# Performance work log

Measured on AMD Instinct MI355X. Metric: run time of the kernel, lower is better.

## Reference

```python
import jax, jax.numpy as jnp
import numpy as np

D = 768          # wav2vec2-base hidden size
H = 4            # cross-attn heads
HD = D // H
B = 8
N = 1024         # w2v sequence length (target length)
T = 2000         # raw CQCC frames
N_GAT = 3
NUM_CLASSES = 2


def _p(key, shape, scale=0.02):
    return jax.random.normal(key, shape, dtype=jnp.float32) * scale


def layer_norm(x, g, b, eps=1e-5):
    m = x.mean(-1, keepdims=True)
    v = x.var(-1, keepdims=True)
    return (x - m) * jax.lax.rsqrt(v + eps) * g + b


def gelu(x):
    return jax.nn.gelu(x, approximate=False)


def conv1d(x, w, b):
    # x [B,C,T], w [O,I,K], padding=1 (same)
    y = jax.lax.conv_general_dilated(x, w, (1,), [(1, 1)], dimension_numbers=('NCH', 'OIH', 'NCH'))
    return y + b[None, :, None]


def batchnorm(x, g, b, m, v, eps=1e-5):
    # eval-mode BatchNorm1d on [B,C,T]
    return (x - m[None, :, None]) * jax.lax.rsqrt(v[None, :, None] + eps) * g[None, :, None] + b[None, :, None]


def interp_linear(x, target_len):
    # torch F.interpolate(mode='linear', align_corners=False); x [B,T,D] -> [B,target_len,D]
    t_in = x.shape[1]
    pos = (jnp.arange(target_len, dtype=jnp.float32) + 0.5) * (t_in / target_len) - 0.5
    pos = jnp.clip(pos, 0.0, t_in - 1.0)
    lo = jnp.floor(pos).astype(jnp.int32)
    hi = jnp.minimum(lo + 1, t_in - 1)
    w = (pos - lo.astype(jnp.float32))[None, :, None]
    return x[:, lo] * (1.0 - w) + x[:, hi] * w


def mha(q, k, v, in_w, in_b, out_w, out_b):
    # torch nn.MultiheadAttention, batch_first=True
    bb, nq, _ = q.shape
    nk = k.shape[1]
    wq, wk, wv = in_w[:D], in_w[D:2 * D], in_w[2 * D:]
    bq, bk, bv = in_b[:D], in_b[D:2 * D], in_b[2 * D:]
    qh = (q @ wq.T + bq).reshape(bb, nq, H, HD).transpose(0, 2, 1, 3)
    kh = (k @ wk.T + bk).reshape(bb, nk, H, HD).transpose(0, 2, 1, 3)
    vh = (v @ wv.T + bv).reshape(bb, nk, H, HD).transpose(0, 2, 1, 3)
    scores = jnp.einsum('bhqd,bhkd->bhqk', qh, kh) * (1.0 / np.sqrt(HD))
    alpha = jax.nn.softmax(scores, axis=-1)
    o = jnp.einsum('bhqk,bhkd->bhqd', alpha, vh).transpose(0, 2, 1, 3).reshape(bb, nq, D)
    return o @ out_w.T + out_b


def graph_attn(x, fc_w, fc_b, a_w, a_b):
    # GAT score on concat([h_i, h_j]) decomposes additively: e_ij = a_i.h_i + a_j.h_j + b
    h = x @ fc_w.T + fc_b                      # [B,N,D]
    s_i = h @ a_w[:D]                          # [B,N]
    s_j = h @ a_w[D:]                          # [B,N]
    e = s_i[:, :, None] + s_j[:, None, :] + a_b  # [B,N,N]
    alpha = jax.nn.softmax(e, axis=-1)
    return jnp.einsum('bij,bjd->bid', alpha, h)


def _forward(w2v, cqcc, conv1_w, conv1_b, bn1_g, bn1_b, bn1_m, bn1_v,
             conv2_w, conv2_b, bn2_g, bn2_b, bn2_m, bn2_v, pos_embed,
             lnq_g, lnq_b, lnkv_g, lnkv_b,
             a1_in_w, a1_in_b, a1_out_w, a1_out_b,
             a2_in_w, a2_in_b, a2_out_w, a2_out_b,
             gat_fc_w, gat_fc_b, gat_a_w, gat_a_b, gln_g, gln_b,
             clf_w1, clf_b1, clf_w2, clf_b2):
    # CQCC conv stack
    x = gelu(batchnorm(conv1d(cqcc, conv1_w, conv1_b), bn1_g, bn1_b, bn1_m, bn1_v))
    x = gelu(batchnorm(conv1d(x, conv2_w, conv2_b), bn2_g, bn2_b, bn2_m, bn2_v))  # [B,D,T]
    cq = interp_linear(x.transpose(0, 2, 1), w2v.shape[1])  # [B,N,D]
    # shared positional encoding
    n = w2v.shape[1]
    w = w2v + pos_embed[:, :n]
    cq = cq + pos_embed[:, :n]
    # bidirectional cross attention (norm_q / norm_kv shared across directions)
    out1 = mha(layer_norm(cq, lnq_g, lnq_b), layer_norm(w, lnkv_g, lnkv_b),
               layer_norm(w, lnkv_g, lnkv_b), a1_in_w, a1_in_b, a1_out_w, a1_out_b)
    out2 = mha(layer_norm(w, lnq_g, lnq_b), layer_norm(cq, lnkv_g, lnkv_b),
               layer_norm(cq, lnkv_g, lnkv_b), a2_in_w, a2_in_b, a2_out_w, a2_out_b)
    x = out1 + out2
    # 3 residual graph-attention blocks
    for l in range(N_GAT):
        res = x
        x = graph_attn(x, gat_fc_w[l], gat_fc_b[l], gat_a_w[l], gat_a_b[l])
        x = layer_norm(x + res, gln_g[l], gln_b[l])
    pooled = x.mean(axis=1)
    h = gelu(pooled @ clf_w1.T + clf_b1)
    return h @ clf_w2.T + clf_b2


def setup_inputs():
    ks = iter(jax.random.split(jax.random.key(0), 64))
    inp = {}
    inp['w2v'] = jax.random.normal(next(ks), (B, N, D), dtype=jnp.float32)
    inp['cqcc'] = jax.random.normal(next(ks), (B, 20, T), dtype=jnp.float32)
    inp['conv1_w'] = _p(next(ks), (128, 20, 3)); inp['conv1_b'] = jnp.zeros((128,), jnp.float32)
    inp['bn1_g'] = jnp.ones((128,), jnp.float32); inp['bn1_b'] = jnp.zeros((128,), jnp.float32)
    inp['bn1_m'] = jnp.zeros((128,), jnp.float32); inp['bn1_v'] = jnp.ones((128,), jnp.float32)
    inp['conv2_w'] = _p(next(ks), (D, 128, 3)); inp['conv2_b'] = jnp.zeros((D,), jnp.float32)
    inp['bn2_g'] = jnp.ones((D,), jnp.float32); inp['bn2_b'] = jnp.zeros((D,), jnp.float32)
    inp['bn2_m'] = jnp.zeros((D,), jnp.float32); inp['bn2_v'] = jnp.ones((D,), jnp.float32)
    inp['pos_embed'] = _p(next(ks), (1, 2000, D), 1.0)
    inp['lnq_g'] = jnp.ones((D,), jnp.float32); inp['lnq_b'] = jnp.zeros((D,), jnp.float32)
    inp['lnkv_g'] = jnp.ones((D,), jnp.float32); inp['lnkv_b'] = jnp.zeros((D,), jnp.float32)
    inp['a1_in_w'] = _p(next(ks), (3 * D, D)); inp['a1_in_b'] = jnp.zeros((3 * D,), jnp.float32)
    inp['a1_out_w'] = _p(next(ks), (D, D)); inp['a1_out_b'] = jnp.zeros((D,), jnp.float32)
    inp['a2_in_w'] = _p(next(ks), (3 * D, D)); inp['a2_in_b'] = jnp.zeros((3 * D,), jnp.float32)
    inp['a2_out_w'] = _p(next(ks), (D, D)); inp['a2_out_b'] = jnp.zeros((D,), jnp.float32)
    inp['gat_fc_w'] = _p(next(ks), (N_GAT, D, D)); inp['gat_fc_b'] = jnp.zeros((N_GAT, D), jnp.float32)
    inp['gat_a_w'] = _p(next(ks), (N_GAT, 2 * D)); inp['gat_a_b'] = jnp.zeros((N_GAT,), jnp.float32)
    inp['gln_g'] = jnp.ones((N_GAT, D), jnp.float32); inp['gln_b'] = jnp.zeros((N_GAT, D), jnp.float32)
    inp['clf_w1'] = _p(next(ks), (128, D)); inp['clf_b1'] = jnp.zeros((128,), jnp.float32)
    inp['clf_w2'] = _p(next(ks), (NUM_CLASSES, 128)); inp['clf_b2'] = jnp.zeros((NUM_CLASSES,), jnp.float32)
    return inp


def reference(w2v, cqcc, conv1_w, conv1_b, bn1_g, bn1_b, bn1_m, bn1_v,
              conv2_w, conv2_b, bn2_g, bn2_b, bn2_m, bn2_v, pos_embed,
              lnq_g, lnq_b, lnkv_g, lnkv_b,
              a1_in_w, a1_in_b, a1_out_w, a1_out_b,
              a2_in_w, a2_in_b, a2_out_w, a2_out_b,
              gat_fc_w, gat_fc_b, gat_a_w, gat_a_b, gln_g, gln_b,
              clf_w1, clf_b1, clf_w2, clf_b2):
    return _forward(w2v, cqcc, conv1_w, conv1_b, bn1_g, bn1_b, bn1_m, bn1_v,
                    conv2_w, conv2_b, bn2_g, bn2_b, bn2_m, bn2_v, pos_embed,
                    lnq_g, lnq_b, lnkv_g, lnkv_b,
                    a1_in_w, a1_in_b, a1_out_w, a1_out_b,
                    a2_in_w, a2_in_b, a2_out_w, a2_out_b,
                    gat_fc_w, gat_fc_b, gat_a_w, gat_a_b, gln_g, gln_b,
                    clf_w1, clf_b1, clf_w2, clf_b2)
```

## Files before the change

### kernel.cpp

```cpp
#include <hip/hip_runtime.h>
#include <math.h>

#define DD 768
#define NH 4
#define HDIM 192
#define BBATCH 8
#define NSEQ 1024
#define TLEN 2000
#define SLOT 6291456
#define XROW 256256

typedef _Float16 h16;
typedef _Float16 half8v __attribute__((ext_vector_type(8)));
typedef _Float16 half4v __attribute__((ext_vector_type(4)));
typedef float f32x4 __attribute__((ext_vector_type(4)));

__device__ __forceinline__ float gelu_f(float x){
  return 0.5f * x * (1.0f + erff(x * 0.70710678118654752440f));
}
__device__ __forceinline__ float wave_sum(float v){
  #pragma unroll
  for (int off = 32; off; off >>= 1) v += __shfl_xor(v, off);
  return v;
}
__device__ __forceinline__ float wave_max(float v){
  #pragma unroll
  for (int off = 32; off; off >>= 1) v = fmaxf(v, __shfl_xor(v, off));
  return v;
}
__device__ __forceinline__ void gload16(const h16* g, h16* l){
  __builtin_amdgcn_global_load_lds(
      (const __attribute__((address_space(1))) void*)g,
      (__attribute__((address_space(3))) void*)l, 16, 0, 0);
}
__device__ __forceinline__ int xcd_remap(int orig, int nwg){
  int q = nwg >> 3, r = nwg & 7;
  int xcd = orig & 7, idx = orig >> 3;
  return (xcd < r ? xcd * (q + 1) : r * (q + 1) + (xcd - r) * q) + idx;
}

struct CastArgs {
  const float* s[5];
  h16* d[5];
  int cum[6];
};
__global__ __launch_bounds__(256) void k_cast5(CastArgs a, int total){
  int i = blockIdx.x * 256 + threadIdx.x;
  if (i >= total) return;
  int seg = 0;
  #pragma unroll
  for (int t = 1; t < 5; ++t) seg += (i >= a.cum[t]);
  int off = i - a.cum[seg];
  a.d[seg][off] = (h16)a.s[seg][off];
}

__global__ __launch_bounds__(256) void k_castc2(const float* __restrict__ s,
    h16* __restrict__ d){
  int i = blockIdx.x * 256 + threadIdx.x;
  if (i >= 294912) return;
  int oc = i / 384, rem = i % 384;
  int ic = rem / 3, kh = rem % 3;
  d[oc * 384 + kh * 128 + ic] = (h16)s[i];
}

__global__ __launch_bounds__(256) void k_conv1t(const float* __restrict__ cqcc,
    const float* __restrict__ w, const float* __restrict__ bias,
    const float* __restrict__ g, const float* __restrict__ be,
    const float* __restrict__ mm, const float* __restrict__ vv,
    h16* __restrict__ X){
  __shared__ float xs[20][258];
  __shared__ float wsm[32*60];
  const int t0 = blockIdx.x * 256;
  const int ocg = blockIdx.y, b = blockIdx.z;
  const int tid = threadIdx.x;
  for (int idx = tid; idx < 20*258; idx += 256){
    int ic = idx / 258, tt = idx % 258;
    int t = t0 + tt - 1;
    xs[ic][tt] = (t >= 0 && t < TLEN) ? cqcc[((size_t)b*20 + ic)*TLEN + t] : 0.f;
  }
  for (int idx = tid; idx < 32*60; idx += 256)
    wsm[idx] = w[ocg*32*60 + idx];
  __syncthreads();
  int t = t0 + tid;
  if (t >= TLEN) return;
  float acc[32] = {};
  for (int ic = 0; ic < 20; ++ic){
    float x0 = xs[ic][tid], x1v = xs[ic][tid+1], x2v = xs[ic][tid+2];
    #pragma unroll
    for (int oc = 0; oc < 32; ++oc){
      const float* wp = &wsm[(oc*20 + ic)*3];
      acc[oc] += wp[0]*x0 + wp[1]*x1v + wp[2]*x2v;
    }
  }
  h16* dst = X + (size_t)b*XROW + (size_t)(t+1)*128 + ocg*32;
  #pragma unroll 4
  for (int oc = 0; oc < 32; ++oc){
    int c = ocg*32 + oc;
    float s = rsqrtf(vv[c] + 1e-5f) * g[c];
    float val = (acc[oc] + bias[c] - mm[c]) * s + be[c];
    dst[oc] = (h16)gelu_f(val);
  }
  if (t == 0){
    h16* z = X + (size_t)b*XROW + ocg*32;
    #pragma unroll
    for (int oc = 0; oc < 32; ++oc) z[oc] = (h16)0.f;
  }
  if (t == TLEN-1){
    h16* z = X + (size_t)b*XROW + (size_t)2001*128 + ocg*32;
    #pragma unroll
    for (int oc = 0; oc < 32; ++oc) z[oc] = (h16)0.f;
  }
}

__global__ void k_bnprep(const float* __restrict__ cb, const float* __restrict__ g,
    const float* __restrict__ be, const float* __restrict__ m,
    const float* __restrict__ v, float* __restrict__ sc, float* __restrict__ off){
  int i = blockIdx.x * 256 + threadIdx.x;
  if (i >= DD) return;
  float s = g[i] * rsqrtf(v[i] + 1e-5f);
  sc[i] = s;
  off[i] = (cb[i] - m[i]) * s + be[i];
}

__global__ __launch_bounds__(256) void k_interp_ln(const h16* __restrict__ x2,
    const float* __restrict__ pe,
    const float* __restrict__ g1, const float* __restrict__ b1, h16* __restrict__ o1,
    const float* __restrict__ g2, const float* __restrict__ b2, h16* __restrict__ o2){
  __shared__ float ss[4], sqq[4];
  int row = blockIdx.x, tid = threadIdx.x;
  int b = row >> 10, i = row & 1023;
  float p = (i + 0.5f) * ((float)TLEN / (float)NSEQ) - 0.5f;
  p = fminf(fmaxf(p, 0.f), (float)(TLEN - 1));
  int lo = (int)floorf(p);
  int hi = min(lo + 1, TLEN - 1);
  float w = p - (float)lo;
  const h16* blo = x2 + ((size_t)b * TLEN + lo) * DD;
  const h16* bhi = x2 + ((size_t)b * TLEN + hi) * DD;
  const float* per = pe + (size_t)i * DD;
  float v[3]; float s = 0.f, sq = 0.f;
  #pragma unroll
  for (int j = 0; j < 3; ++j){
    int d = j * 256 + tid;
    float x = (float)blo[d] * (1.f - w) + (float)bhi[d] * w + per[d];
    v[j] = x; s += x; sq += x * x;
  }
  s = wave_sum(s); sq = wave_sum(sq);
  int wv = tid >> 6;
  if ((tid & 63) == 0){ ss[wv] = s; sqq[wv] = sq; }
  __syncthreads();
  s  = ss[0] + ss[1] + ss[2] + ss[3];
  sq = sqq[0] + sqq[1] + sqq[2] + sqq[3];
  float mean = s * (1.f / DD);
  float var  = sq * (1.f / DD) - mean * mean;
  float r = rsqrtf(var + 1e-5f);
  #pragma unroll
  for (int j = 0; j < 3; ++j){
    int d = j * 256 + tid;
    float xn = (v[j] - mean) * r;
    o1[(size_t)row * DD + d] = (h16)(xn * g1[d] + b1[d]);
    o2[(size_t)row * DD + d] = (h16)(xn * g2[d] + b2[d]);
  }
}

__global__ __launch_bounds__(256) void k_addpos_ln(const float* __restrict__ xin,
    const float* __restrict__ pe,
    const float* __restrict__ g1, const float* __restrict__ b1, h16* __restrict__ o1,
    const float* __restrict__ g2, const float* __restrict__ b2, h16* __restrict__ o2){
  __shared__ float ss[4], sqq[4];
  int row = blockIdx.x, tid = threadIdx.x;
  int i = row & 1023;
  const float* ip = xin + (size_t)row * DD;
  const float* per = pe + (size_t)i * DD;
  float v[3]; float s = 0.f, sq = 0.f;
  #pragma unroll
  for (int j = 0; j < 3; ++j){
    int d = j * 256 + tid;
    float x = ip[d] + per[d];
    v[j] = x; s += x; sq += x * x;
  }
  s = wave_sum(s); sq = wave_sum(sq);
  int wv = tid >> 6;
  if ((tid & 63) == 0){ ss[wv] = s; sqq[wv] = sq; }
  __syncthreads();
  s  = ss[0] + ss[1] + ss[2] + ss[3];
  sq = sqq[0] + sqq[1] + sqq[2] + sqq[3];
  float mean = s * (1.f / DD);
  float var  = sq * (1.f / DD) - mean * mean;
  float r = rsqrtf(var + 1e-5f);
  #pragma unroll
  for (int j = 0; j < 3; ++j){
    int d = j * 256 + tid;
    float xn = (v[j] - mean) * r;
    o1[(size_t)row * DD + d] = (h16)(xn * g1[d] + b1[d]);
    o2[(size_t)row * DD + d] = (h16)(xn * g2[d] + b2[d]);
  }
}

__global__ __launch_bounds__(256) void k_lnH(const h16* __restrict__ in,
    const float* __restrict__ ctx, const float* __restrict__ g,
    const float* __restrict__ be, h16* __restrict__ out){
  __shared__ float ss[4], sqq[4];
  int row = blockIdx.x, tid = threadIdx.x;
  const h16* ip = in + (size_t)row * DD;
  int b = row >> 10;
  float v[3]; float s = 0.f, sq = 0.f;
  #pragma unroll
  for (int j = 0; j < 3; ++j){
    int d = j * 256 + tid;
    float x = (float)ip[d] + ctx[b * DD + d];
    v[j] = x; s += x; sq += x * x;
  }
  s = wave_sum(s); sq = wave_sum(sq);
  int w = tid >> 6;
  if ((tid & 63) == 0){ ss[w] = s; sqq[w] = sq; }
  __syncthreads();
  s  = ss[0] + ss[1] + ss[2] + ss[3];
  sq = sqq[0] + sqq[1] + sqq[2] + sqq[3];
  float mean = s * (1.f / DD);
  float var  = sq * (1.f / DD) - mean * mean;
  float r = rsqrtf(var + 1e-5f);
  #pragma unroll
  for (int j = 0; j < 3; ++j){
    int d = j * 256 + tid;
    out[(size_t)row * DD + d] = (h16)((v[j] - mean) * r * g[d] + be[d]);
  }
}

#define GEMM_MAINLOOP(Abase, lda, Wbase, ldw, Kdim)                          \
  auto stage = [&](int buf, int kt){                                         \
    _Pragma("unroll")                                                        \
    for (int i = 0; i < 4; ++i){                                             \
      int p = i*256 + tid; int row = p >> 3; int ch = (p & 7) ^ (row & 7);   \
      gload16(Abase + (size_t)(m0+row)*lda + kt + ch*8, &Als[buf][p*8]);     \
    }                                                                        \
    _Pragma("unroll")                                                        \
    for (int i = 0; i < 4; ++i){                                             \
      int p = i*256 + tid; int row = p >> 3; int ch = (p & 7) ^ (row & 7);   \
      gload16(Wbase + (size_t)(n0+row)*ldw + kt + ch*8, &Bls[buf][p*8]);     \
    }                                                                        \
  };                                                                         \
  stage(0, 0);                                                               \
  const int nk = Kdim >> 6;                                                  \
  for (int t = 0; t < nk; ++t){                                              \
    const int cur = t & 1;                                                   \
    if (t + 1 < nk){                                                         \
      stage(cur ^ 1, (t + 1) << 6);                                          \
      asm volatile("s_waitcnt vmcnt(8)" ::: "memory");                       \
    } else {                                                                 \
      asm volatile("s_waitcnt vmcnt(0)" ::: "memory");                       \
    }                                                                        \
    __builtin_amdgcn_s_barrier();                                            \
    __builtin_amdgcn_sched_barrier(0);                                       \
    __builtin_amdgcn_s_setprio(1);                                           \
    _Pragma("unroll")                                                        \
    for (int kk = 0; kk < 2; ++kk){                                          \
      half8v af[4], bf[4];                                                   \
      _Pragma("unroll")                                                      \
      for (int mi = 0; mi < 4; ++mi){                                        \
        int row = wr*64 + mi*16 + lr;                                        \
        int chp = (kk*4 + lg) ^ (row & 7);                                   \
        af[mi] = *(const half8v*)&Als[cur][row*64 + chp*8];                  \
      }                                                                      \
      _Pragma("unroll")                                                      \
      for (int ni = 0; ni < 4; ++ni){                                        \
        int row = wc*64 + ni*16 + lr;                                        \
        int chp = (kk*4 + lg) ^ (row & 7);                                   \
        bf[ni] = *(const half8v*)&Bls[cur][row*64 + chp*8];                  \
      }                                                                      \
      _Pragma("unroll")                                                      \
      for (int mi = 0; mi < 4; ++mi)                                         \
        _Pragma("unroll")                                                    \
        for (int ni = 0; ni < 4; ++ni)                                       \
          acc[mi][ni] = __builtin_amdgcn_mfma_f32_16x16x32_f16(              \
              af[mi], bf[ni], acc[mi][ni], 0, 0, 0);                         \
    }                                                                        \
    __builtin_amdgcn_s_setprio(0);                                           \
    asm volatile("s_waitcnt lgkmcnt(0)" ::: "memory");                       \
    __builtin_amdgcn_sched_barrier(0);                                       \
    __builtin_amdgcn_s_barrier();                                            \
  }

__global__ __launch_bounds__(256) void k_gemm_h(
    const h16* __restrict__ A, const h16* __restrict__ W,
    int lda, int ldw, int ldc, int K,
    const float* __restrict__ bias, const float* __restrict__ sc,
    const float* __restrict__ off, const h16* __restrict__ addh,
    float* __restrict__ outf, h16* __restrict__ outh,
    const float* __restrict__ rdw, float* __restrict__ rdpart)
{
  __shared__ h16 Als[2][128*64];
  __shared__ h16 Bls[2][128*64];
  const int tid = threadIdx.x;
  const int gx = gridDim.x, gy = gridDim.y;
  const int wg = xcd_remap(blockIdx.x + gx * blockIdx.y, gx * gy);
  const int nidx = wg % gx;
  const int n0 = nidx * 128, m0 = (wg / gx) * 128;
  const int lane = tid & 63, wid = tid >> 6;
  const int wr = wid >> 1, wc = wid & 1;
  const int lr = lane & 15, lg = lane >> 4;
  f32x4 acc[4][4] = {};
  GEMM_MAINLOOP(A, lda, W, ldw, K)
  float rd[4][4] = {};
  #pragma unroll
  for (int mi = 0; mi < 4; ++mi){
    #pragma unroll
    for (int ni = 0; ni < 4; ++ni){
      int col = n0 + wc*64 + ni*16 + lr;
      int rowb = m0 + wr*64 + mi*16 + lg*4;
      float cb = bias ? bias[col] : 0.f;
      float aw = rdw ? rdw[col] : 0.f;
      #pragma unroll
      for (int r = 0; r < 4; ++r){
        size_t idx = (size_t)(rowb + r) * ldc + col;
        float v = acc[mi][ni][r];
        if (sc){ v = v * sc[col] + off[col]; v = gelu_f(v); }
        else v += cb;
        if (addh) v += (float)addh[idx];
        if (outf) outf[idx] = v;
        if (outh) outh[idx] = (h16)v;
        if (rdw) rd[mi][r] += v * aw;
      }
    }
  }
  if (rdw){
    #pragma unroll
    for (int mi = 0; mi < 4; ++mi){
      #pragma unroll
      for (int r = 0; r < 4; ++r){
        float p = rd[mi][r];
        #pragma unroll
        for (int o = 1; o < 16; o <<= 1) p += __shfl_xor(p, o);
        if (lr == 0){
          int row = m0 + wr*64 + mi*16 + lg*4 + r;
          rdpart[(size_t)row * 12 + nidx*2 + wc] = p;
        }
      }
    }
  }
}

__global__ __launch_bounds__(256) void k_conv2g(
    const h16* __restrict__ X, const h16* __restrict__ W,
    const float* __restrict__ sc, const float* __restrict__ off,
    h16* __restrict__ out)
{
  __shared__ h16 Als[2][128*64];
  __shared__ h16 Bls[2][128*64];
  const int tid = threadIdx.x;
  const int gx = gridDim.x, gy = gridDim.y;
  const int wg = xcd_remap(blockIdx.x + gx * blockIdx.y, gx * gy);
  const int n0 = (wg % gx) * 128, m0 = (wg / gx) * 128;
  const int lane = tid & 63, wid = tid >> 6;
  const int wr = wid >> 1, wc = wid & 1;
  const int lr = lane & 15, lg = lane >> 4;
  f32x4 acc[4][4] = {};
  auto stage = [&](int buf, int kt){
    #pragma unroll
    for (int i = 0; i < 4; ++i){
      int p = i*256 + tid; int row = p >> 3; int ch = (p & 7) ^ (row & 7);
      int rm = m0 + row, b = rm >> 11, t = rm & 2047;
      gload16(X + (size_t)b*XROW + (size_t)t*128 + kt + ch*8, &Als[buf][p*8]);
    }
    #pragma unroll
    for (int i = 0; i < 4; ++i){
      int p = i*256 + tid; int row = p >> 3; int ch = (p & 7) ^ (row & 7);
      gload16(W + (size_t)(n0+row)*384 + kt + ch*8, &Bls[buf][p*8]);
    }
  };
  stage(0, 0);
  const int nk = 6;
  for (int t = 0; t < nk; ++t){
    const int cur = t & 1;
    if (t + 1 < nk){
      stage(cur ^ 1, (t + 1) << 6);
      asm volatile("s_waitcnt vmcnt(8)" ::: "memory");
    } else {
      asm volatile("s_waitcnt vmcnt(0)" ::: "memory");
    }
    __builtin_amdgcn_s_barrier();
    __builtin_amdgcn_sched_barrier(0);
    __builtin_amdgcn_s_setprio(1);
    #pragma unroll
    for (int kk = 0; kk < 2; ++kk){
      half8v af[4], bf[4];
      #pragma unroll
      for (int mi = 0; mi < 4; ++mi){
        int row = wr*64 + mi*16 + lr;
        int chp = (kk*4 + lg) ^ (row & 7);
        af[mi] = *(const half8v*)&Als[cur][row*64 + chp*8];
      }
      #pragma unroll
      for (int ni = 0; ni < 4; ++ni){
        int row = wc*64 + ni*16 + lr;
        int chp = (kk*4 + lg) ^ (row & 7);
        bf[ni] = *(const half8v*)&Bls[cur][row*64 + chp*8];
      }
      #pragma unroll
      for (int mi = 0; mi < 4; ++mi)
        #pragma unroll
        for (int ni = 0; ni < 4; ++ni)
          acc[mi][ni] = __builtin_amdgcn_mfma_f32_16x16x32_f16(
              af[mi], bf[ni], acc[mi][ni], 0, 0, 0);
    }
    __builtin_amdgcn_s_setprio(0);
    asm volatile("s_waitcnt lgkmcnt(0)" ::: "memory");
    __builtin_amdgcn_sched_barrier(0);
    __builtin_amdgcn_s_barrier();
  }
  #pragma unroll
  for (int mi = 0; mi < 4; ++mi){
    #pragma unroll
    for (int ni = 0; ni < 4; ++ni){
      int col = n0 + wc*64 + ni*16 + lr;
      int rowb = m0 + wr*64 + mi*16 + lg*4;
      #pragma unroll
      for (int r = 0; r < 4; ++r){
        int rm = rowb + r, b = rm >> 11, t = rm & 2047;
        if (t < TLEN){
          float v = acc[mi][ni][r] * sc[col] + off[col];
          out[((size_t)b*TLEN + t)*DD + col] = (h16)gelu_f(v);
        }
      }
    }
  }
}

__global__ __launch_bounds__(256) void k_gemm6(
    const h16* __restrict__ Lall, const h16* __restrict__ w6,
    const float* __restrict__ b1, const float* __restrict__ b2,
    h16* __restrict__ qkv6)
{
  __shared__ h16 Als[2][128*64];
  __shared__ h16 Bls[2][128*64];
  const int tid = threadIdx.x;
  const int gx = gridDim.x, gy = gridDim.y;
  const int nwg = gx * gy * 6;
  const int wg = xcd_remap(blockIdx.x + gx*(blockIdx.y + gy*blockIdx.z), nwg);
  const int n0 = (wg % gx) * 128;
  const int m0 = ((wg / gx) % gy) * 128;
  const int bz = wg / (gx * gy);
  const int aidx = (1468 >> (2*bz)) & 3;
  const h16* A = Lall + (size_t)aidx * SLOT;
  const h16* W = w6 + (size_t)bz * 589824;
  const float* bias = (bz < 3 ? b1 + bz*DD : b2 + (bz-3)*DD);
  h16* C = qkv6 + (size_t)bz * SLOT;
  const int lane = tid & 63, wid = tid >> 6;
  const int wr = wid >> 1, wc = wid & 1;
  const int lr = lane & 15, lg = lane >> 4;
  f32x4 acc[4][4] = {};
  GEMM_MAINLOOP(A, DD, W, DD, DD)
  #pragma unroll
  for (int mi = 0; mi < 4; ++mi){
    #pragma unroll
    for (int ni = 0; ni < 4; ++ni){
      int col = n0 + wc*64 + ni*16 + lr;
      int rowb = m0 + wr*64 + mi*16 + lg*4;
      float cb = bias[col];
      #pragma unroll
      for (int r = 0; r < 4; ++r)
        C[(size_t)(rowb + r) * DD + col] = (h16)(acc[mi][ni][r] + cb);
    }
  }
}

__global__ __launch_bounds__(256) void k_trV(const h16* __restrict__ Vh, int ldv,
    h16* __restrict__ VT){
  __shared__ h16 tile[64*64];
  const int z = blockIdx.z, b = z >> 2, h = z & 3;
  const int q0 = blockIdx.x * 64, d0 = blockIdx.y * 64;
  const int t = threadIdx.x;
  {
    int qq = t >> 2, ds = (t & 3) * 16;
    const h16* src = Vh + ((size_t)b*NSEQ + q0 + qq)*ldv + h*HDIM + d0 + ds;
    half8v v0 = *(const half8v*)src;
    half8v v1 = *(const half8v*)(src + 8);
    int c0 = (ds >> 3) ^ (qq & 7), c1 = ((ds >> 3) + 1) ^ (qq & 7);
    *(half8v*)&tile[qq*64 + c0*8] = v0;
    *(half8v*)&tile[qq*64 + c1*8] = v1;
  }
  __syncthreads();
  {
    int dd = t >> 2, qs = (t & 3) * 16;
    half8v o0, o1;
    #pragma unroll
    for (int j = 0; j < 8; ++j){
      int q = qs + j, q2 = qs + 8 + j;
      o0[j] = tile[q*64  + (((dd>>3) ^ (q&7))*8)  + (dd & 7)];
      o1[j] = tile[q2*64 + (((dd>>3) ^ (q2&7))*8) + (dd & 7)];
    }
    h16* dst = VT + (size_t)z*HDIM*NSEQ + (size_t)(d0+dd)*NSEQ + q0 + qs;
    *(half8v*)dst = o0;
    *(half8v*)(dst + 8) = o1;
  }
}

__global__ __launch_bounds__(256) void k_flash(const h16* __restrict__ Qp,
    const h16* __restrict__ Kp, const h16* __restrict__ VTp,
    h16* __restrict__ Op){
  __shared__ h16 Ks[2][32*192];
  __shared__ h16 Vs[2][192*32];
  __shared__ h16 Ps[4][16*32];
  const int tid = threadIdx.x;
  const int bh = blockIdx.x, qt = blockIdx.y;
  const int b = bh >> 2, h = bh & 3;
  const int q0 = qt * 64;
  const h16* Qg = Qp + (size_t)b*NSEQ*DD + h*HDIM;
  const h16* Kg = Kp + (size_t)b*NSEQ*DD + h*HDIM;
  const h16* Vg = VTp + (size_t)bh*HDIM*NSEQ;
  const int lane = tid & 63, wid = tid >> 6;
  const int lr = lane & 15, lg = lane >> 4;
  half8v qf[6];
  {
    int qrow = q0 + wid*16 + lr;
    #pragma unroll
    for (int ks = 0; ks < 6; ++ks)
      qf[ks] = *(const half8v*)(Qg + (size_t)qrow*DD + ks*32 + lg*8);
  }
  auto stageK = [&](int buf, int k0){
    #pragma unroll
    for (int i = 0; i < 3; ++i){
      int p = i*256 + tid;
      int row = p / 24, chp = p % 24;
      int ch = chp ^ (row & 7);
      gload16(Kg + (size_t)(k0+row)*DD + ch*8, &Ks[buf][p*8]);
    }
  };
  auto stageV = [&](int buf, int k0){
    #pragma unroll
    for (int i = 0; i < 3; ++i){
      int p = i*256 + tid;
      int row = p >> 2, chp = p & 3;
      int ch = chp ^ ((row >> 1) & 3);
      gload16(Vg + (size_t)row*NSEQ + k0 + ch*8, &Vs[buf][p*8]);
    }
  };
  stageK(0, 0); stageV(0, 0);
  f32x4 oacc[12] = {};
  float m_run[4] = {-1e30f, -1e30f, -1e30f, -1e30f};
  float l_run[4] = {};
  const float SC = 0.07216878364870322f;
  __syncthreads();
  for (int kt = 0; kt < 32; ++kt){
    const int cur = kt & 1;
    if (kt + 1 < 32){ stageK(cur^1, (kt+1)*32); stageV(cur^1, (kt+1)*32); }
    f32x4 sacc[2] = {};
    __builtin_amdgcn_s_setprio(1);
    #pragma unroll
    for (int ks = 0; ks < 6; ++ks){
      #pragma unroll
      for (int t = 0; t < 2; ++t){
        int krow = t*16 + lr;
        int ch = (ks*4 + lg) ^ (krow & 7);
        half8v kf = *(const half8v*)&Ks[cur][krow*192 + ch*8];
        sacc[t] = __builtin_amdgcn_mfma_f32_16x16x32_f16(qf[ks], kf, sacc[t], 0, 0, 0);
      }
    }
    __builtin_amdgcn_s_setprio(0);
    float mnew[4], c[4], psum[4];
    #pragma unroll
    for (int r = 0; r < 4; ++r){
      float mt = fmaxf(sacc[0][r], sacc[1][r]);
      #pragma unroll
      for (int off = 1; off < 16; off <<= 1) mt = fmaxf(mt, __shfl_xor(mt, off));
      mnew[r] = fmaxf(m_run[r], mt * SC);
      c[r] = __expf(m_run[r] - mnew[r]);
      psum[r] = 0.f;
    }
    #pragma unroll
    for (int t = 0; t < 2; ++t){
      #pragma unroll
      for (int r = 0; r < 4; ++r){
        float p = __expf(sacc[t][r] * SC - mnew[r]);
        psum[r] += p;
        int q = lg*4 + r, key = t*16 + lr;
        int ch = (t*2 + (lr>>3)) ^ ((q>>1) & 3);
        Ps[wid][q*32 + ch*8 + (key & 7)] = (h16)p;
      }
    }
    #pragma unroll
    for (int r = 0; r < 4; ++r){
      #pragma unroll
      for (int off = 1; off < 16; off <<= 1) psum[r] += __shfl_xor(psum[r], off);
      l_run[r] = l_run[r] * c[r] + psum[r];
      m_run[r] = mnew[r];
    }
    #pragma unroll
    for (int dt = 0; dt < 12; ++dt){
      f32x4 o = oacc[dt];
      o[0] *= c[0]; o[1] *= c[1]; o[2] *= c[2]; o[3] *= c[3];
      oacc[dt] = o;
    }
    asm volatile("s_waitcnt lgkmcnt(0)" ::: "memory");
    __builtin_amdgcn_sched_barrier(0);
    {
      int pch = lg ^ ((lr >> 1) & 3);
      half8v pf = *(const half8v*)&Ps[wid][lr*32 + pch*8];
      __builtin_amdgcn_s_setprio(1);
      #pragma unroll
      for (int dt = 0; dt < 12; ++dt){
        int drow = dt*16 + lr;
        int vch = lg ^ ((drow >> 1) & 3);
        half8v vf = *(const half8v*)&Vs[cur][drow*32 + vch*8];
        oacc[dt] = __builtin_amdgcn_mfma_f32_16x16x32_f16(pf, vf, oacc[dt], 0, 0, 0);
      }
      __builtin_amdgcn_s_setprio(0);
    }
    __syncthreads();
  }
  float inv[4];
  #pragma unroll
  for (int r = 0; r < 4; ++r) inv[r] = 1.0f / l_run[r];
  h16* Og = Op + (size_t)b*NSEQ*DD + h*HDIM;
  #pragma unroll
  for (int dt = 0; dt < 12; ++dt){
    #pragma unroll
    for (int r = 0; r < 4; ++r){
      int q = q0 + wid*16 + lg*4 + r;
      Og[(size_t)q*DD + dt*16 + lr] = (h16)(oacc[dt][r] * inv[r]);
    }
  }
}

__global__ __launch_bounds__(256) void k_softmax12(const float* __restrict__ part,
    float* __restrict__ y){
  __shared__ float red[4];
  int b = blockIdx.x, tid = threadIdx.x;
  float v[4]; float mx = -1e30f;
  #pragma unroll
  for (int j = 0; j < 4; ++j){
    int i = j * 256 + tid;
    const float* p = part + (size_t)(b * NSEQ + i) * 12;
    float s = 0.f;
    #pragma unroll
    for (int k = 0; k < 12; ++k) s += p[k];
    v[j] = s; mx = fmaxf(mx, s);
  }
  mx = wave_max(mx);
  if ((tid & 63) == 0) red[tid >> 6] = mx;
  __syncthreads();
  mx = fmaxf(fmaxf(red[0], red[1]), fmaxf(red[2], red[3]));
  __syncthreads();
  float s = 0.f;
  #pragma unroll
  for (int j = 0; j < 4; ++j){ v[j] = __expf(v[j] - mx); s += v[j]; }
  s = wave_sum(s);
  if ((tid & 63) == 0) red[tid >> 6] = s;
  __syncthreads();
  s = red[0] + red[1] + red[2] + red[3];
  float inv = 1.0f / s;
  #pragma unroll
  for (int j = 0; j < 4; ++j) y[b * NSEQ + j * 256 + tid] = v[j] * inv;
}

__global__ __launch_bounds__(256) void k_ctx1(const float* __restrict__ alpha,
    const h16* __restrict__ h, float* __restrict__ part){
  int d = blockIdx.x * 256 + threadIdx.x;
  int b = blockIdx.y, pc = blockIdx.z;
  if (d >= DD) return;
  float acc = 0.f;
  const h16* hp = h + ((size_t)b * NSEQ + pc * 64) * DD + d;
  const float* ap = alpha + b * NSEQ + pc * 64;
  #pragma unroll 4
  for (int j = 0; j < 64; ++j) acc += ap[j] * (float)hp[(size_t)j * DD];
  part[(size_t)(b * 16 + pc) * DD + d] = acc;
}
__global__ __launch_bounds__(256) void k_ctx2(const float* __restrict__ part,
    float scale, float* __restrict__ ctx){
  int d = blockIdx.x * 256 + threadIdx.x;
  int b = blockIdx.y;
  if (d >= DD) return;
  float acc = 0.f;
  #pragma unroll
  for (int p = 0; p < 16; ++p) acc += part[(size_t)(b * 16 + p) * DD + d];
  ctx[b * DD + d] = acc * scale;
}

__global__ __launch_bounds__(256) void k_pool1(const h16* __restrict__ x,
    float* __restrict__ part){
  int d = blockIdx.x * 256 + threadIdx.x;
  int b = blockIdx.y, pc = blockIdx.z;
  if (d >= DD) return;
  float acc = 0.f;
  const h16* xp = x + ((size_t)b * NSEQ + pc * 64) * DD + d;
  #pragma unroll 4
  for (int j = 0; j < 64; ++j) acc += (float)xp[(size_t)j * DD];
  part[(size_t)(b * 16 + pc) * DD + d] = acc;
}

__global__ __launch_bounds__(128) void k_clf(const float* __restrict__ pooled,
    const float* __restrict__ w1, const float* __restrict__ b1,
    const float* __restrict__ w2, const float* __restrict__ b2,
    float* __restrict__ out){
  __shared__ float pl[DD];
  __shared__ float h1[128];
  int b = blockIdx.x, tid = threadIdx.x;
  #pragma unroll
  for (int j = 0; j < 6; ++j) pl[j * 128 + tid] = pooled[b * DD + j * 128 + tid];
  __syncthreads();
  float acc = b1[tid];
  const float* wp = w1 + (size_t)tid * DD;
  for (int d = 0; d < DD; ++d) acc += pl[d] * wp[d];
  h1[tid] = gelu_f(acc);
  __syncthreads();
  if (tid < 2){
    float o = b2[tid];
    const float* w2p = w2 + tid * 128;
    for (int c = 0; c < 128; ++c) o += h1[c] * w2p[c];
    out[b * 2 + tid] = o;
  }
}

extern "C" void kernel_launch(void* const* d_in, const int* in_sizes, int n_in,
                              void* d_out, int out_size, void* d_ws, size_t ws_size,
                              hipStream_t stream){
  (void)in_sizes; (void)n_in; (void)out_size;
  const float* w2v      = (const float*)d_in[0];
  const float* cqcc     = (const float*)d_in[1];
  const float* conv1_w  = (const float*)d_in[2];
  const float* conv1_b  = (const float*)d_in[3];
  const float* bn1_g    = (const float*)d_in[4];
  const float* bn1_b    = (const float*)d_in[5];
  const float* bn1_m    = (const float*)d_in[6];
  const float* bn1_v    = (const float*)d_in[7];
  const float* conv2_w  = (const float*)d_in[8];
  const float* conv2_b  = (const float*)d_in[9];
  const float* bn2_g    = (const float*)d_in[10];
  const float* bn2_b    = (const float*)d_in[11];
  const float* bn2_m    = (const float*)d_in[12];
  const float* bn2_v    = (const float*)d_in[13];
  const float* pos_embed= (const float*)d_in[14];
  const float* lnq_g    = (const float*)d_in[15];
  const float* lnq_b    = (const float*)d_in[16];
  const float* lnkv_g   = (const float*)d_in[17];
  const float* lnkv_b   = (const float*)d_in[18];
  const float* a1_in_w  = (const float*)d_in[19];
  const float* a1_in_b  = (const float*)d_in[20];
  const float* a1_out_w = (const float*)d_in[21];
  const float* a1_out_b = (const float*)d_in[22];
  const float* a2_in_w  = (const float*)d_in[23];
  const float* a2_in_b  = (const float*)d_in[24];
  const float* a2_out_w = (const float*)d_in[25];
  const float* a2_out_b = (const float*)d_in[26];
  const float* gat_fc_w = (const float*)d_in[27];
  const float* gat_fc_b = (const float*)d_in[28];
  const float* gat_a_w  = (const float*)d_in[29];
  const float* gln_g    = (const float*)d_in[31];
  const float* gln_b    = (const float*)d_in[32];
  const float* clf_w1   = (const float*)d_in[33];
  const float* clf_b1   = (const float*)d_in[34];
  const float* clf_w2   = (const float*)d_in[35];
  const float* clf_b2   = (const float*)d_in[36];

  char* wsp = (char*)d_ws;
  auto F = [&](size_t bytes){ char* p = wsp; wsp += (bytes + 255) & ~(size_t)255; return p; };
  h16* xh      = (h16*)F(12582912);
  h16* Lall    = (h16*)F(4*12582912);
  h16* qkv6    = (h16*)F(6*12582912);
  h16* VT      = (h16*)F(12582912);
  h16* o1h     = (h16*)F(12582912);
  h16* w6      = (h16*)F(2*3538944);
  h16* w_a1out = (h16*)F(1179648);
  h16* w_a2out = (h16*)F(1179648);
  h16* w_gat   = (h16*)F(3538944);
  h16* w_c2    = (h16*)F(589824);
  float* scb   = (float*)F(3072);
  float* offb  = (float*)F(3072);
  float* alpha = (float*)F(32768);
  float* ctxb  = (float*)F(24576);
  float* pooled= (float*)F(24576);
  float* partb = (float*)F(393216);
  if ((size_t)(wsp - (char*)d_ws) > ws_size) return;

  h16* X   = Lall;
  h16* x2h = qkv6;
  h16* hh  = qkv6;

  const int NR = BBATCH * NSEQ;

  {
    CastArgs ca;
    ca.s[0]=a1_in_w;  ca.d[0]=w6;            int n0=1769472;
    ca.s[1]=a2_in_w;  ca.d[1]=w6+1769472;    int n1=1769472;
    ca.s[2]=a1_out_w; ca.d[2]=w_a1out;       int n2=589824;
    ca.s[3]=a2_out_w; ca.d[3]=w_a2out;       int n3=589824;
    ca.s[4]=gat_fc_w; ca.d[4]=w_gat;         int n4=1769472;
    ca.cum[0]=0; ca.cum[1]=n0; ca.cum[2]=n0+n1; ca.cum[3]=n0+n1+n2;
    ca.cum[4]=n0+n1+n2+n3; ca.cum[5]=n0+n1+n2+n3+n4;
    int total = ca.cum[5];
    k_cast5<<<(total+255)/256, 256, 0, stream>>>(ca, total);
  }
  k_castc2<<<(294912+255)/256, 256, 0, stream>>>(conv2_w, w_c2);
  k_bnprep<<<3, 256, 0, stream>>>(conv2_b, bn2_g, bn2_b, bn2_m, bn2_v, scb, offb);

  k_conv1t<<<dim3(8, 4, BBATCH), 256, 0, stream>>>(cqcc, conv1_w, conv1_b,
      bn1_g, bn1_b, bn1_m, bn1_v, X);
  k_conv2g<<<dim3(6, 128), 256, 0, stream>>>(X, w_c2, scb, offb, x2h);

  k_interp_ln<<<NR, 256, 0, stream>>>(x2h, pos_embed,
      lnq_g, lnq_b, Lall, lnkv_g, lnkv_b, Lall + SLOT);
  k_addpos_ln<<<NR, 256, 0, stream>>>(w2v, pos_embed,
      lnq_g, lnq_b, Lall + 2*SLOT, lnkv_g, lnkv_b, Lall + 3*SLOT);

  k_gemm6<<<dim3(6, 64, 6), 256, 0, stream>>>(Lall, w6, a1_in_b, a2_in_b, qkv6);

  dim3 gflash(32, 16);

  k_trV<<<dim3(16, 3, 32), 256, 0, stream>>>(qkv6 + 2*(size_t)SLOT, DD, VT);
  k_flash<<<gflash, 256, 0, stream>>>(qkv6, qkv6 + (size_t)SLOT, VT, qkv6);
  k_gemm_h<<<dim3(6, 64), 256, 0, stream>>>(qkv6, w_a1out, DD, DD, DD, DD,
      a1_out_b, nullptr, nullptr, nullptr, nullptr, o1h, nullptr, nullptr);

  k_trV<<<dim3(16, 3, 32), 256, 0, stream>>>(qkv6 + 5*(size_t)SLOT, DD, VT);
  k_flash<<<gflash, 256, 0, stream>>>(qkv6 + 3*(size_t)SLOT, qkv6 + 4*(size_t)SLOT,
                                      VT, qkv6 + 3*(size_t)SLOT);
  k_gemm_h<<<dim3(6, 64), 256, 0, stream>>>(qkv6 + 3*(size_t)SLOT, w_a2out,
      DD, DD, DD, DD, a2_out_b, nullptr, nullptr, o1h, nullptr, xh, nullptr, nullptr);

  for (int l = 0; l < 3; ++l){
    k_gemm_h<<<dim3(6, 64), 256, 0, stream>>>(xh, w_gat + (size_t)l*589824,
        DD, DD, DD, DD, gat_fc_b + l*DD, nullptr, nullptr, nullptr,
        nullptr, hh, gat_a_w + l*2*DD + DD, partb);
    k_softmax12<<<BBATCH, 256, 0, stream>>>(partb, alpha);
    k_ctx1<<<dim3(3, BBATCH, 16), 256, 0, stream>>>(alpha, hh, partb);
    k_ctx2<<<dim3(3, BBATCH), 256, 0, stream>>>(partb, 1.0f, ctxb);
    k_lnH<<<NR, 256, 0, stream>>>(xh, ctxb, gln_g + l*DD, gln_b + l*DD, xh);
  }

  k_pool1<<<dim3(3, BBATCH, 16), 256, 0, stream>>>(xh, partb);
  k_ctx2<<<dim3(3, BBATCH), 256, 0, stream>>>(partb, 1.0f/NSEQ, pooled);
  k_clf<<<BBATCH, 128, 0, stream>>>(pooled, clf_w1, clf_b1, clf_w2, clf_b2,
                                    (float*)d_out);
}
```

Measured before the change: 631.6 us.

## Batch both cross-attention branches into single transpose, flash and out-proj launches

The two independent cross-attention branches now share one V-transpose launch, one flash-attention launch with a z dimension, and one batched output-projection GEMM, instead of running sequentially as separate kernels. This doubles the grid of each launch to fill more compute units and cuts launch count and tail effects. In exchange it adds a separate fp16 elementwise add kernel to sum the two projections, extra workspace buffers, and an extra write and read of two activation tensors. The unused epilogue branches of the generic GEMM are also removed.

```diff
diff --git a/kernel.cpp b/kernel.cpp
--- a/kernel.cpp
+++ b/kernel.cpp
@@ -223,6 +223,16 @@
   for (int j = 0; j < 3; ++j){
     int d = j * 256 + tid;
     out[(size_t)row * DD + d] = (h16)((v[j] - mean) * r * g[d] + be[d]);
+  }
+}
+
+__global__ __launch_bounds__(256) void k_addh(const h16* __restrict__ a,
+    const h16* __restrict__ b, h16* __restrict__ o, int n8){
+  int i = blockIdx.x * 256 + threadIdx.x;
+  if (i < n8){
+    half8v x = ((const half8v*)a)[i];
+    half8v y = ((const half8v*)b)[i];
+    ((half8v*)o)[i] = x + y;
   }
 }
 
@@ -283,9 +293,8 @@
 __global__ __launch_bounds__(256) void k_gemm_h(
     const h16* __restrict__ A, const h16* __restrict__ W,
     int lda, int ldw, int ldc, int K,
-    const float* __restrict__ bias, const float* __restrict__ sc,
-    const float* __restrict__ off, const h16* __restrict__ addh,
-    float* __restrict__ outf, h16* __restrict__ outh,
+    const float* __restrict__ bias,
+    h16* __restrict__ outh,
     const float* __restrict__ rdw, float* __restrict__ rdpart)
 {
   __shared__ h16 Als[2][128*64];
@@ -307,17 +316,13 @@
     for (int ni = 0; ni < 4; ++ni){
       int col = n0 + wc*64 + ni*16 + lr;
       int rowb = m0 + wr*64 + mi*16 + lg*4;
-      float cb = bias ? bias[col] : 0.f;
+      float cb = bias[col];
       float aw = rdw ? rdw[col] : 0.f;
       #pragma unroll
       for (int r = 0; r < 4; ++r){
         size_t idx = (size_t)(rowb + r) * ldc + col;
-        float v = acc[mi][ni][r];
-        if (sc){ v = v * sc[col] + off[col]; v = gelu_f(v); }
-        else v += cb;
-        if (addh) v += (float)addh[idx];
-        if (outf) outf[idx] = v;
-        if (outh) outh[idx] = (h16)v;
+        float v = acc[mi][ni][r] + cb;
+        outh[idx] = (h16)v;
         if (rdw) rd[mi][r] += v * aw;
       }
     }
@@ -335,6 +340,44 @@
           rdpart[(size_t)row * 12 + nidx*2 + wc] = p;
         }
       }
+    }
+  }
+}
+
+__global__ __launch_bounds__(256) void k_gemmop(
+    const h16* __restrict__ A0, const h16* __restrict__ A1,
+    const h16* __restrict__ W0, const h16* __restrict__ W1,
+    const float* __restrict__ bb0, const float* __restrict__ bb1,
+    h16* __restrict__ C0, h16* __restrict__ C1)
+{
+  __shared__ h16 Als[2][128*64];
+  __shared__ h16 Bls[2][128*64];
+  const int tid = threadIdx.x;
+  const int gx = gridDim.x, gy = gridDim.y;
+  const int nwg = gx * gy * 2;
+  const int wg = xcd_remap(blockIdx.x + gx*(blockIdx.y + gy*blockIdx.z), nwg);
+  const int n0 = (wg % gx) * 128;
+  const int m0 = ((wg / gx) % gy) * 128;
+  const int bz = wg / (gx * gy);
+  const h16* A = bz ? A1 : A0;
+  const h16* W = bz ? W1 : W0;
+  const float* bias = bz ? bb1 : bb0;
+  h16* C = bz ? C1 : C0;
+  const int lane = tid & 63, wid = tid >> 6;
+  const int wr = wid >> 1, wc = wid & 1;
+  const int lr = lane & 15, lg = lane >> 4;
+  f32x4 acc[4][4] = {};
+  GEMM_MAINLOOP(A, DD, W, DD, DD)
+  #pragma unroll
+  for (int mi = 0; mi < 4; ++mi){
+    #pragma unroll
+    for (int ni = 0; ni < 4; ++ni){
+      int col = n0 + wc*64 + ni*16 + lr;
+      int rowb = m0 + wr*64 + mi*16 + lg*4;
+      float cb = bias[col];
+      #pragma unroll
+      for (int r = 0; r < 4; ++r)
+        C[(size_t)(rowb + r) * DD + col] = (h16)(acc[mi][ni][r] + cb);
     }
   }
 }
@@ -463,15 +506,19 @@
   }
 }
 
-__global__ __launch_bounds__(256) void k_trV(const h16* __restrict__ Vh, int ldv,
-    h16* __restrict__ VT){
+__global__ __launch_bounds__(256) void k_trV(const h16* __restrict__ V0,
+    const h16* __restrict__ V1, h16* __restrict__ VT0, h16* __restrict__ VT1){
   __shared__ h16 tile[64*64];
-  const int z = blockIdx.z, b = z >> 2, h = z & 3;
+  const int zz = blockIdx.z;
+  const int which = zz >> 5, bh = zz & 31;
+  const int b = bh >> 2, h = bh & 3;
+  const h16* Vh = which ? V1 : V0;
+  h16* VT = which ? VT1 : VT0;
   const int q0 = blockIdx.x * 64, d0 = blockIdx.y * 64;
   const int t = threadIdx.x;
   {
     int qq = t >> 2, ds = (t & 3) * 16;
-    const h16* src = Vh + ((size_t)b*NSEQ + q0 + qq)*ldv + h*HDIM + d0 + ds;
+    const h16* src = Vh + ((size_t)b*NSEQ + q0 + qq)*DD + h*HDIM + d0 + ds;
     half8v v0 = *(const half8v*)src;
     half8v v1 = *(const half8v*)(src + 8);
     int c0 = (ds >> 3) ^ (qq & 7), c1 = ((ds >> 3) + 1) ^ (qq & 7);
@@ -488,22 +535,28 @@
       o0[j] = tile[q*64  + (((dd>>3) ^ (q&7))*8)  + (dd & 7)];
       o1[j] = tile[q2*64 + (((dd>>3) ^ (q2&7))*8) + (dd & 7)];
     }
-    h16* dst = VT + (size_t)z*HDIM*NSEQ + (size_t)(d0+dd)*NSEQ + q0 + qs;
+    h16* dst = VT + (size_t)bh*HDIM*NSEQ + (size_t)(d0+dd)*NSEQ + q0 + qs;
     *(half8v*)dst = o0;
     *(half8v*)(dst + 8) = o1;
   }
 }
 
-__global__ __launch_bounds__(256) void k_flash(const h16* __restrict__ Qp,
-    const h16* __restrict__ Kp, const h16* __restrict__ VTp,
-    h16* __restrict__ Op){
+__global__ __launch_bounds__(256) void k_flash(
+    const h16* __restrict__ Q0, const h16* __restrict__ K0,
+    const h16* __restrict__ T0, h16* __restrict__ O0,
+    const h16* __restrict__ Q1, const h16* __restrict__ K1,
+    const h16* __restrict__ T1, h16* __restrict__ O1){
   __shared__ h16 Ks[2][32*192];
   __shared__ h16 Vs[2][192*32];
   __shared__ h16 Ps[4][16*32];
   const int tid = threadIdx.x;
-  const int bh = blockIdx.x, qt = blockIdx.y;
+  const int bh = blockIdx.x, qt = blockIdx.y, which = blockIdx.z;
   const int b = bh >> 2, h = bh & 3;
   const int q0 = qt * 64;
+  const h16* Qp = which ? Q1 : Q0;
+  const h16* Kp = which ? K1 : K0;
+  const h16* VTp = which ? T1 : T0;
+  h16* Op = which ? O1 : O0;
   const h16* Qg = Qp + (size_t)b*NSEQ*DD + h*HDIM;
   const h16* Kg = Kp + (size_t)b*NSEQ*DD + h*HDIM;
   const h16* Vg = VTp + (size_t)bh*HDIM*NSEQ;
@@ -757,7 +810,9 @@
   h16* Lall    = (h16*)F(4*12582912);
   h16* qkv6    = (h16*)F(6*12582912);
   h16* VT      = (h16*)F(12582912);
+  h16* VT2     = (h16*)F(12582912);
   h16* o1h     = (h16*)F(12582912);
+  h16* o2h     = (h16*)F(12582912);
   h16* w6      = (h16*)F(2*3538944);
   h16* w_a1out = (h16*)F(1179648);
   h16* w_a2out = (h16*)F(1179648);
@@ -803,23 +858,20 @@
 
   k_gemm6<<<dim3(6, 64, 6), 256, 0, stream>>>(Lall, w6, a1_in_b, a2_in_b, qkv6);
 
-  dim3 gflash(32, 16);
-
-  k_trV<<<dim3(16, 3, 32), 256, 0, stream>>>(qkv6 + 2*(size_t)SLOT, DD, VT);
-  k_flash<<<gflash, 256, 0, stream>>>(qkv6, qkv6 + (size_t)SLOT, VT, qkv6);
-  k_gemm_h<<<dim3(6, 64), 256, 0, stream>>>(qkv6, w_a1out, DD, DD, DD, DD,
-      a1_out_b, nullptr, nullptr, nullptr, nullptr, o1h, nullptr, nullptr);
-
-  k_trV<<<dim3(16, 3, 32), 256, 0, stream>>>(qkv6 + 5*(size_t)SLOT, DD, VT);
-  k_flash<<<gflash, 256, 0, stream>>>(qkv6 + 3*(size_t)SLOT, qkv6 + 4*(size_t)SLOT,
-                                      VT, qkv6 + 3*(size_t)SLOT);
-  k_gemm_h<<<dim3(6, 64), 256, 0, stream>>>(qkv6 + 3*(size_t)SLOT, w_a2out,
-      DD, DD, DD, DD, a2_out_b, nullptr, nullptr, o1h, nullptr, xh, nullptr, nullptr);
+  k_trV<<<dim3(16, 3, 64), 256, 0, stream>>>(qkv6 + 2*(size_t)SLOT,
+      qkv6 + 5*(size_t)SLOT, VT, VT2);
+  k_flash<<<dim3(32, 16, 2), 256, 0, stream>>>(
+      qkv6, qkv6 + (size_t)SLOT, VT, qkv6,
+      qkv6 + 3*(size_t)SLOT, qkv6 + 4*(size_t)SLOT, VT2,
+      qkv6 + 3*(size_t)SLOT);
+  k_gemmop<<<dim3(6, 64, 2), 256, 0, stream>>>(
+      qkv6, qkv6 + 3*(size_t)SLOT, w_a1out, w_a2out,
+      a1_out_b, a2_out_b, o1h, o2h);
+  k_addh<<<(NR*DD/8 + 255)/256, 256, 0, stream>>>(o1h, o2h, xh, NR*DD/8);
 
   for (int l = 0; l < 3; ++l){
     k_gemm_h<<<dim3(6, 64), 256, 0, stream>>>(xh, w_gat + (size_t)l*589824,
-        DD, DD, DD, DD, gat_fc_b + l*DD, nullptr, nullptr, nullptr,
-        nullptr, hh, gat_a_w + l*2*DD + DD, partb);
+        DD, DD, DD, DD, gat_fc_b + l*DD, hh, gat_a_w + l*2*DD + DD, partb);
     k_softmax12<<<BBATCH, 256, 0, stream>>>(partb, alpha);
     k_ctx1<<<dim3(3, BBATCH, 16), 256, 0, stream>>>(alpha, hh, partb);
     k_ctx2<<<dim3(3, BBATCH), 256, 0, stream>>>(partb, 1.0f, ctxb);
```

Measured after the change: 582.6 us. 7.8% less time.
